# Optimization experiments

Hardware: AMD Instinct MI355X
Metric: run time of the kernel (lower is better)

The kernel has to match this reference:

```python
import jax, jax.numpy as jnp
import numpy as np

N_NODES = 100000
N_EDGES = 3200000
NCLASSES = 4
IN_DIM = 2          # per-node feature dim -> edge in_feats = 2*IN_DIM = 4
HID = 8             # output_dim


def setup_inputs() -> dict:
    key = jax.random.key(0)
    k_m, k_e, k_w1, k_b1, k_w2, k_b2 = jax.random.split(key, 6)
    m = jax.random.normal(k_m, (N_NODES, NCLASSES, IN_DIM), dtype=jnp.float32)
    edge_index = jax.random.randint(k_e, (2, N_EDGES), 0, N_NODES, dtype=jnp.int64)
    in_feats = 2 * IN_DIM
    # ClasswiseLinear: one independent Linear per class (grouped weights)
    s1 = 1.0 / np.sqrt(in_feats)
    s2 = 1.0 / np.sqrt(HID)
    W1 = jax.random.uniform(k_w1, (NCLASSES, in_feats, HID), jnp.float32, -s1, s1)
    b1 = jax.random.uniform(k_b1, (NCLASSES, HID), jnp.float32, -s1, s1)
    W2 = jax.random.uniform(k_w2, (NCLASSES, HID, 1), jnp.float32, -s2, s2)
    b2 = jax.random.uniform(k_b2, (NCLASSES, 1), jnp.float32, -s2, s2)
    return {"m": m, "edge_index": edge_index, "W1": W1, "b1": b1, "W2": W2, "b2": b2}


def reference(m, edge_index, W1, b1, W2, b2):
    row, col = edge_index[0], edge_index[1]
    # gather node features per edge; concat dest/src -> [E, C, 2*IN_DIM]
    B = jnp.concatenate([m[col], m[row]], axis=-1)
    B = jax.lax.stop_gradient(B)  # original code calls .detach()
    # classwise linear 1 + tanh: grouped GEMM over class axis c
    h = jnp.tanh(jnp.einsum("eci,cih->ech", B, W1) + b1)      # [E, C, HID]
    o = jnp.tanh(jnp.einsum("ech,cho->eco", h, W2) + b2)      # [E, C, 1]
    # softmax over the class dimension (dim=1)
    return jax.nn.softmax(o, axis=1)
```

## Files before the change

kernel.cpp:

```cpp
#include <hip/hip_runtime.h>

#define TWO_LOG2E 2.8853901817779268f
#define LOG2E     1.4426950408889634f

typedef float f32x2 __attribute__((ext_vector_type(2)));
typedef float f32x4 __attribute__((ext_vector_type(4)));

template<int CTRL>
__device__ __forceinline__ float dpp_qperm(float x) {
    int r = __builtin_amdgcn_update_dpp(0, __float_as_int(x), CTRL, 0xF, 0xF, true);
    return __int_as_float(r);
}

__global__ __launch_bounds__(256) void edge_mlp(
    const float* __restrict__ m,
    const int*   __restrict__ eidx,
    const float* __restrict__ W1,
    const float* __restrict__ b1,
    const float* __restrict__ W2,
    const float* __restrict__ b2,
    float*       __restrict__ out,
    const int nE)
{
    __shared__ __align__(16) float sw1[128];
    __shared__ __align__(8)  float sbw[64];
    __shared__ float so0[4];

    const int tidb = threadIdx.x;
    if (tidb < 128) {
        const int c = tidb >> 5, q = tidb & 31, j = q >> 2, i = q & 3;
        sw1[tidb] = W1[c * 32 + i * 8 + j] * TWO_LOG2E;
    } else if (tidb < 192) {
        const int q = tidb - 128, c = q >> 4, r = q & 15, j = r >> 1;
        sbw[q] = (r & 1) ? W2[c * 8 + j] * (-2.0f * TWO_LOG2E)
                         : b1[c * 8 + j] * TWO_LOG2E;
    } else if (tidb < 196) {
        const int c = tidb - 192;
        float s = b2[c];
        #pragma unroll
        for (int j = 0; j < 8; ++j) s += W2[c * 8 + j];
        so0[c] = s * TWO_LOG2E;
    }
    __syncthreads();

    const int tid0 = blockIdx.x * blockDim.x + threadIdx.x;
    const int c = tid0 & 3;
    const int cc2 = c * 2;
    const float* w1c = sw1 + c * 32;
    const float* bwc = sbw + c * 16;
    const float o0 = so0[c];

    const int* eidx1 = eidx + nE;
    const int total  = nE * 4;
    const int stride = gridDim.x * blockDim.x;

    constexpr int UN = 4;
    int t = tid0;

    for (; t + (UN - 1) * stride < total; t += UN * stride) {
        int row[UN], col[UN];
        #pragma unroll
        for (int k = 0; k < UN; ++k) {
            const int e = (t + k * stride) >> 2;
            row[k] = __builtin_nontemporal_load(eidx  + e);
            col[k] = __builtin_nontemporal_load(eidx1 + e);
        }
        f32x2 mc[UN], mr[UN];
        #pragma unroll
        for (int k = 0; k < UN; ++k) {
            mc[k] = *(const f32x2*)(m + (unsigned)col[k] * 8u + cc2);
            mr[k] = *(const f32x2*)(m + (unsigned)row[k] * 8u + cc2);
        }
        #pragma unroll
        for (int k = 0; k < UN; ++k) {
            float o = o0;
            #pragma unroll
            for (int j = 0; j < 8; j += 2) {
                const f32x4 Wa  = *(const f32x4*)(w1c + j * 4);
                const f32x4 Wb  = *(const f32x4*)(w1c + j * 4 + 4);
                const f32x2 bwa = *(const f32x2*)(bwc + j * 2);
                const f32x2 bwb = *(const f32x2*)(bwc + j * 2 + 2);
                float h0 = bwa.x, h1 = bwb.x;
                h0 = fmaf(mc[k].x, Wa.x, h0);  h1 = fmaf(mc[k].x, Wb.x, h1);
                h0 = fmaf(mc[k].y, Wa.y, h0);  h1 = fmaf(mc[k].y, Wb.y, h1);
                h0 = fmaf(mr[k].x, Wa.z, h0);  h1 = fmaf(mr[k].x, Wb.z, h1);
                h0 = fmaf(mr[k].y, Wa.w, h0);  h1 = fmaf(mr[k].y, Wb.w, h1);
                const float a0 = __builtin_amdgcn_exp2f(h0) + 1.0f;
                const float a1 = __builtin_amdgcn_exp2f(h1) + 1.0f;
                const float inv = __builtin_amdgcn_rcpf(a0 * a1);
                o = fmaf(bwa.y, inv * a1, o);
                o = fmaf(bwb.y, inv * a0, o);
            }
            const float e2 = __builtin_amdgcn_exp2f(o);
            const float r2 = __builtin_amdgcn_rcpf(e2 + 1.0f);
            const float y  = fmaf(-2.0f, r2, 1.0f);
            float p = fmaf(y, 0.0013888889f, 0.0083333333f);
            p = fmaf(p, y, 0.0416666667f);
            p = fmaf(p, y, 0.1666666667f);
            p = fmaf(p, y, 0.5f);
            p = fmaf(p, y, 1.0f);
            p = fmaf(p, y, 1.0f);
            float s = p + dpp_qperm<0xB1>(p);
            s = s + dpp_qperm<0x4E>(s);
            __builtin_nontemporal_store(p * __builtin_amdgcn_rcpf(s),
                                        out + (t + k * stride));
        }
    }

    for (; t < total; t += stride) {
        const int e  = t >> 2;
        const int r0 = eidx[e];
        const int c0 = eidx1[e];
        const f32x2 mcv = *(const f32x2*)(m + (unsigned)c0 * 8u + cc2);
        const f32x2 mrv = *(const f32x2*)(m + (unsigned)r0 * 8u + cc2);
        float o = o0;
        #pragma unroll
        for (int j = 0; j < 8; j += 2) {
            const f32x4 Wa  = *(const f32x4*)(w1c + j * 4);
            const f32x4 Wb  = *(const f32x4*)(w1c + j * 4 + 4);
            const f32x2 bwa = *(const f32x2*)(bwc + j * 2);
            const f32x2 bwb = *(const f32x2*)(bwc + j * 2 + 2);
            float h0 = bwa.x, h1 = bwb.x;
            h0 = fmaf(mcv.x, Wa.x, h0);  h1 = fmaf(mcv.x, Wb.x, h1);
            h0 = fmaf(mcv.y, Wa.y, h0);  h1 = fmaf(mcv.y, Wb.y, h1);
            h0 = fmaf(mrv.x, Wa.z, h0);  h1 = fmaf(mrv.x, Wb.z, h1);
            h0 = fmaf(mrv.y, Wa.w, h0);  h1 = fmaf(mrv.y, Wb.w, h1);
            const float a0 = __builtin_amdgcn_exp2f(h0) + 1.0f;
            const float a1 = __builtin_amdgcn_exp2f(h1) + 1.0f;
            const float inv = __builtin_amdgcn_rcpf(a0 * a1);
            o = fmaf(bwa.y, inv * a1, o);
            o = fmaf(bwb.y, inv * a0, o);
        }
        const float e2 = __builtin_amdgcn_exp2f(o);
        const float r2 = __builtin_amdgcn_rcpf(e2 + 1.0f);
        const float y  = fmaf(-2.0f, r2, 1.0f);
        float p = fmaf(y, 0.0013888889f, 0.0083333333f);
        p = fmaf(p, y, 0.0416666667f);
        p = fmaf(p, y, 0.1666666667f);
        p = fmaf(p, y, 0.5f);
        p = fmaf(p, y, 1.0f);
        p = fmaf(p, y, 1.0f);
        float s = p + dpp_qperm<0xB1>(p);
        s = s + dpp_qperm<0x4E>(s);
        out[t] = p * __builtin_amdgcn_rcpf(s);
    }
}

extern "C" void kernel_launch(void* const* d_in, const int* in_sizes, int n_in,
                              void* d_out, int out_size, void* d_ws, size_t ws_size,
                              hipStream_t stream) {
    const float* m  = (const float*)d_in[0];
    const int* eidx = (const int*)d_in[1];
    const float* W1 = (const float*)d_in[2];
    const float* b1 = (const float*)d_in[3];
    const float* W2 = (const float*)d_in[4];
    const float* b2 = (const float*)d_in[5];
    float* out = (float*)d_out;
    const int nE = in_sizes[1] / 2;

    const int threads = 256;
    const int blocks  = 2048;
    hipLaunchKernelGGL(edge_mlp, dim3(blocks), dim3(threads), 0, stream,
                       m, eidx, W1, b1, W2, b2, out, nE);
}
```

Baseline: 56.48 us.

## Software-pipeline index and gather loads across loop iterations; pad LDS weight rows

Restructures the main unrolled loop into a software pipeline. Edge indices for the next iteration are loaded before the current compute, and node feature gathers are issued after the current stores, so memory latency overlaps with transcendental math. It also pads the per-class shared-memory weight arrays (stride 36 and 18) to avoid LDS bank conflicts between the four class lanes. The cost is higher register pressure from the extra in-flight buffers, which may lower occupancy.

```diff
diff --git a/kernel.cpp b/kernel.cpp
--- a/kernel.cpp
+++ b/kernel.cpp
@@ -22,20 +22,26 @@
     float*       __restrict__ out,
     const int nE)
 {
-    __shared__ __align__(16) float sw1[128];
-    __shared__ __align__(8)  float sbw[64];
+    __shared__ __align__(16) float sw1[4 * 36];
+    __shared__ __align__(16) float sbw[4 * 18];
     __shared__ float so0[4];
 
     const int tidb = threadIdx.x;
-    if (tidb < 128) {
-        const int c = tidb >> 5, q = tidb & 31, j = q >> 2, i = q & 3;
-        sw1[tidb] = W1[c * 32 + i * 8 + j] * TWO_LOG2E;
-    } else if (tidb < 192) {
-        const int q = tidb - 128, c = q >> 4, r = q & 15, j = r >> 1;
-        sbw[q] = (r & 1) ? W2[c * 8 + j] * (-2.0f * TWO_LOG2E)
-                         : b1[c * 8 + j] * TWO_LOG2E;
-    } else if (tidb < 196) {
-        const int c = tidb - 192;
+    if (tidb < 144) {
+        const int c = tidb / 36, r = tidb % 36;
+        if (r < 32) {
+            const int j = r >> 2, i = r & 3;
+            sw1[tidb] = W1[c * 32 + i * 8 + j] * TWO_LOG2E;
+        }
+    } else if (tidb < 216) {
+        const int q = tidb - 144, c = q / 18, r = q % 18;
+        if (r < 16) {
+            const int j = r >> 1;
+            sbw[q] = (r & 1) ? W2[c * 8 + j] * (-2.0f * TWO_LOG2E)
+                             : b1[c * 8 + j] * TWO_LOG2E;
+        }
+    } else if (tidb < 220) {
+        const int c = tidb - 216;
         float s = b2[c];
         #pragma unroll
         for (int j = 0; j < 8; ++j) s += W2[c * 8 + j];
@@ -46,30 +52,46 @@
     const int tid0 = blockIdx.x * blockDim.x + threadIdx.x;
     const int c = tid0 & 3;
     const int cc2 = c * 2;
-    const float* w1c = sw1 + c * 32;
-    const float* bwc = sbw + c * 16;
+    const float* w1c = sw1 + c * 36;
+    const float* bwc = sbw + c * 18;
     const float o0 = so0[c];
 
     const int* eidx1 = eidx + nE;
     const int total  = nE * 4;
     const int stride = gridDim.x * blockDim.x;
+    constexpr int UN = 4;
+    const int step = UN * stride;
 
-    constexpr int UN = 4;
     int t = tid0;
+    f32x2 mc[UN], mr[UN];
 
-    for (; t + (UN - 1) * stride < total; t += UN * stride) {
-        int row[UN], col[UN];
+    bool have = (t + (UN - 1) * stride < total);
+    if (have) {
+        int row0[UN], col0[UN];
         #pragma unroll
         for (int k = 0; k < UN; ++k) {
             const int e = (t + k * stride) >> 2;
-            row[k] = __builtin_nontemporal_load(eidx  + e);
-            col[k] = __builtin_nontemporal_load(eidx1 + e);
+            row0[k] = __builtin_nontemporal_load(eidx  + e);
+            col0[k] = __builtin_nontemporal_load(eidx1 + e);
         }
-        f32x2 mc[UN], mr[UN];
         #pragma unroll
         for (int k = 0; k < UN; ++k) {
-            mc[k] = *(const f32x2*)(m + (unsigned)col[k] * 8u + cc2);
-            mr[k] = *(const f32x2*)(m + (unsigned)row[k] * 8u + cc2);
+            mc[k] = *(const f32x2*)(m + (unsigned)col0[k] * 8u + cc2);
+            mr[k] = *(const f32x2*)(m + (unsigned)row0[k] * 8u + cc2);
+        }
+    }
+
+    while (have) {
+        const int tn = t + step;
+        const bool haveN = (tn + (UN - 1) * stride < total);
+        int rowN[UN], colN[UN];
+        if (haveN) {
+            #pragma unroll
+            for (int k = 0; k < UN; ++k) {
+                const int e = (tn + k * stride) >> 2;
+                rowN[k] = __builtin_nontemporal_load(eidx  + e);
+                colN[k] = __builtin_nontemporal_load(eidx1 + e);
+            }
         }
         #pragma unroll
         for (int k = 0; k < UN; ++k) {
@@ -105,6 +127,15 @@
             __builtin_nontemporal_store(p * __builtin_amdgcn_rcpf(s),
                                         out + (t + k * stride));
         }
+        if (haveN) {
+            #pragma unroll
+            for (int k = 0; k < UN; ++k) {
+                mc[k] = *(const f32x2*)(m + (unsigned)colN[k] * 8u + cc2);
+                mr[k] = *(const f32x2*)(m + (unsigned)rowN[k] * 8u + cc2);
+            }
+        }
+        t = tn;
+        have = haveN;
     }
 
     for (; t < total; t += stride) {
```

Measured after the change: 56.73 us. About the same (+0.4%).
